# Kernel tuning notes

Hardware: AMD Instinct MI355X
Metric: run time of the kernel (lower is better)

## Reference

```python
import jax, jax.numpy as jnp
import numpy as np

DIM = 1024
HEADS = 16
HIDDEN = 4096
EPS = 1e-5


def layernorm(x, w, b):
    mu = jnp.mean(x, axis=-1, keepdims=True)
    var = jnp.var(x, axis=-1, keepdims=True)
    return (x - mu) * jax.lax.rsqrt(var + EPS) * w + b


def setup_inputs() -> dict:
    key = jax.random.key(0)
    ks = jax.random.split(key, 12)
    s = lambda fan_in: 1.0 / np.sqrt(fan_in)
    return {
        "x": jax.random.normal(ks[0], (8, 1024, DIM), dtype=jnp.float32),
        "norm1_w": jnp.ones((DIM,), jnp.float32),
        "norm1_b": jnp.zeros((DIM,), jnp.float32),
        "qkv_w": jax.random.uniform(ks[1], (3 * DIM, DIM), jnp.float32, -s(DIM), s(DIM)),
        "proj_w": jax.random.uniform(ks[2], (DIM, DIM), jnp.float32, -s(DIM), s(DIM)),
        "proj_b": jax.random.uniform(ks[3], (DIM,), jnp.float32, -s(DIM), s(DIM)),
        "norm2_w": jnp.ones((DIM,), jnp.float32),
        "norm2_b": jnp.zeros((DIM,), jnp.float32),
        "fc1_w": jax.random.uniform(ks[4], (HIDDEN, DIM), jnp.float32, -s(DIM), s(DIM)),
        "fc1_b": jax.random.uniform(ks[5], (HIDDEN,), jnp.float32, -s(DIM), s(DIM)),
        "fc2_w": jax.random.uniform(ks[6], (DIM, HIDDEN), jnp.float32, -s(HIDDEN), s(HIDDEN)),
        "fc2_b": jax.random.uniform(ks[7], (DIM,), jnp.float32, -s(HIDDEN), s(HIDDEN)),
    }


def reference(x, norm1_w, norm1_b, qkv_w, proj_w, proj_b,
              norm2_w, norm2_b, fc1_w, fc1_b, fc2_w, fc2_b):
    B, N, C = x.shape
    hd = C // HEADS
    scale = hd ** -0.5

    # ---- attention branch ----
    xn = layernorm(x, norm1_w, norm1_b)
    qkv_tmp = jnp.einsum('bnc,oc->bno', xn, qkv_w)          # [B,N,3C]
    qkv = qkv_tmp.reshape(B, N, 3, HEADS, hd).transpose(2, 0, 3, 1, 4)
    q, k, v = qkv[0], qkv[1], qkv[2]                         # [B,H,N,hd]
    qkv_out = qkv_tmp.reshape(B, N, 3, C).transpose(2, 0, 1, 3)
    attn = jnp.einsum('bhnd,bhmd->bhnm', q, k) * scale       # [B,H,N,N]
    attn = jax.nn.softmax(attn, axis=-1)
    ao = jnp.einsum('bhnm,bhmd->bhnd', attn, v)              # [B,H,N,hd]
    ao = ao.transpose(0, 2, 1, 3).reshape(B, N, C)
    attn_out = jnp.einsum('bnc,oc->bno', ao, proj_w) + proj_b
    x = x + attn_out

    # ---- mlp branch ----
    xn2 = layernorm(x, norm2_w, norm2_b)
    h = jnp.einsum('bnc,hc->bnh', xn2, fc1_w) + fc1_b
    h = jax.nn.gelu(h, approximate=False)
    hidden_out = jnp.einsum('bnh,ch->bnc', h, fc2_w) + fc2_b
    x = x + hidden_out
    return (x, (qkv_out[0], qkv_out[1], qkv_out[2]), hidden_out)
```

## Files before the change

### kernel.cpp

```cpp
#include <hip/hip_runtime.h>
#include <hip/hip_bf16.h>

typedef __attribute__((ext_vector_type(8))) __bf16 bf16x8;
typedef __attribute__((ext_vector_type(4))) float f32x4;
typedef unsigned short u16;
typedef unsigned int u32;

#define TOK 8192
#define C_DIM 1024
#define OUT_SEC 8388608

__device__ __forceinline__ u16 f2bf(float f) {
  return __builtin_bit_cast(u16, __float2bfloat16(f));
}

__device__ __forceinline__ void gl_lds16(const void* g, void* l) {
  __builtin_amdgcn_global_load_lds(
      (__attribute__((address_space(1))) void*)const_cast<void*>(g),
      (__attribute__((address_space(3))) void*)l, 16, 0, 0);
}

__device__ __forceinline__ float gelu_f(float x) {
  float y = 0.7978845608f * (x + 0.044715f * x * x * x);
  y = fminf(fmaxf(y, -15.f), 15.f);
  float e = __expf(2.0f * y);
  float th = (e - 1.0f) / (e + 1.0f);
  return 0.5f * x * (1.0f + th);
}

__global__ __launch_bounds__(256) void cvt_kernel(const float* __restrict__ in,
                                                  u16* __restrict__ out, int n4) {
  int i = blockIdx.x * blockDim.x + threadIdx.x;
  if (i >= n4) return;
  float4 v = reinterpret_cast<const float4*>(in)[i];
  alignas(8) u16 pk[4];
  pk[0] = f2bf(v.x); pk[1] = f2bf(v.y); pk[2] = f2bf(v.z); pk[3] = f2bf(v.w);
  reinterpret_cast<uint2*>(out)[i] = *reinterpret_cast<uint2*>(pk);
}

__global__ __launch_bounds__(256) void ln_kernel(const float* __restrict__ x,
                                                 const float* __restrict__ w,
                                                 const float* __restrict__ b,
                                                 u16* __restrict__ out) {
  const int row = blockIdx.x;
  const int t = threadIdx.x;
  const float* xr = x + (size_t)row * C_DIM;
  float4 v = reinterpret_cast<const float4*>(xr)[t];
  float s = v.x + v.y + v.z + v.w;
  float ss = v.x * v.x + v.y * v.y + v.z * v.z + v.w * v.w;
#pragma unroll
  for (int off = 1; off < 64; off <<= 1) {
    s += __shfl_xor(s, off, 64);
    ss += __shfl_xor(ss, off, 64);
  }
  __shared__ float red[8];
  const int wv = t >> 6;
  if ((t & 63) == 0) { red[wv] = s; red[4 + wv] = ss; }
  __syncthreads();
  s = red[0] + red[1] + red[2] + red[3];
  ss = red[4] + red[5] + red[6] + red[7];
  const float mu = s * (1.0f / C_DIM);
  const float var = ss * (1.0f / C_DIM) - mu * mu;
  const float rstd = rsqrtf(var + 1e-5f);
  float4 w4 = reinterpret_cast<const float4*>(w)[t];
  float4 b4 = reinterpret_cast<const float4*>(b)[t];
  alignas(8) u16 pk[4];
  pk[0] = f2bf((v.x - mu) * rstd * w4.x + b4.x);
  pk[1] = f2bf((v.y - mu) * rstd * w4.y + b4.y);
  pk[2] = f2bf((v.z - mu) * rstd * w4.z + b4.z);
  pk[3] = f2bf((v.w - mu) * rstd * w4.w + b4.w);
  reinterpret_cast<uint2*>(out + (size_t)row * C_DIM)[t] = *reinterpret_cast<uint2*>(pk);
}

__global__ __launch_bounds__(256) void vtrans_kernel(const float* __restrict__ vsrc,
                                                     u16* __restrict__ vt) {
  const int bh = blockIdx.x, nt = blockIdx.y;
  const int b = bh >> 4, h = bh & 15;
  const int t = threadIdx.x;
  __shared__ u16 T[64][65];
#pragma unroll
  for (int p = 0; p < 4; ++p) {
    const int idx = p * 256 + t;
    const int n = idx >> 4, d4 = (idx & 15) * 4;
    float4 x4 = *reinterpret_cast<const float4*>(
        vsrc + (size_t)(b * 1024 + nt * 64 + n) * 1024 + h * 64 + d4);
    T[d4 + 0][n] = f2bf(x4.x);
    T[d4 + 1][n] = f2bf(x4.y);
    T[d4 + 2][n] = f2bf(x4.z);
    T[d4 + 3][n] = f2bf(x4.w);
  }
  __syncthreads();
  const int d = t >> 2, ns = (t & 3) * 16;
  u16* dst = vt + (size_t)bh * 65536 + (size_t)d * 1024 + nt * 64 + ns;
  alignas(16) u16 tmp[16];
#pragma unroll
  for (int i = 0; i < 16; ++i) tmp[i] = T[d][ns + i];
  reinterpret_cast<uint4*>(dst)[0] = reinterpret_cast<uint4*>(tmp)[0];
  reinterpret_cast<uint4*>(dst)[1] = reinterpret_cast<uint4*>(tmp)[1];
}

enum { EPI8_QKV = 0, EPI8_FC1 = 1 };

#define MFMA_Q(BASE)                                                        \
  _Pragma("unroll") for (int nf = 0; nf < 4; ++nf) {                        \
    _Pragma("unroll") for (int mf = 0; mf < 4; ++mf)                        \
        acc[(BASE) + mf][nf] = __builtin_amdgcn_mfma_f32_16x16x32_bf16(     \
            af[mf], bfr[nf], acc[(BASE) + mf][nf], 0, 0, 0);                \
  }

template <int EPI>
__global__ __launch_bounds__(512, 2) void gemm8(
    const u16* __restrict__ A, const u16* __restrict__ Bw,
    const float* __restrict__ bias,
    float* __restrict__ out, u16* __restrict__ h1, u16* __restrict__ h2,
    int K) {
  extern __shared__ char smem[];
  const int t = threadIdx.x, lane = t & 63, wid = t >> 6;
  const int wm = wid >> 2, wn = wid & 3;

  const int nwg = gridDim.x;
  int lin = blockIdx.x;
  lin = (lin & 7) * (nwg >> 3) + (lin >> 3);
  const int brow0 = (lin & 31) * 256;
  const int bcol0 = (lin >> 5) * 256;

  const int NT = K >> 6;

  f32x4 zero = {0.f, 0.f, 0.f, 0.f};
  f32x4 acc[8][4];
#pragma unroll
  for (int m = 0; m < 8; ++m)
#pragma unroll
    for (int n = 0; n < 4; ++n) acc[m][n] = zero;

  const int src_slot = ((t & 3) ^ ((t >> 3) & 3)) * 8;
  const int srow = t >> 2;
  auto stage = [&](int buf, int mat, int ks, int ktile) {
    const u16* G = mat ? Bw : A;
    const int gr0 = mat ? bcol0 : brow0;
    const int k0 = ktile * 64 + ks * 32 + src_slot;
    char* dst = smem + ((buf << 16) | (mat << 15) | (ks << 14));
#pragma unroll
    for (int i = 0; i < 2; ++i)
      gl_lds16(G + (size_t)(gr0 + i * 128 + srow) * K + k0, dst + i * 8192 + t * 16);
  };

  const int swz16 = (((lane >> 4) ^ ((lane >> 1) & 3)) << 4);
  const int l15 = lane & 15;

  stage(0, 0, 0, 0);
  stage(0, 1, 0, 0);
  stage(0, 0, 1, 0);
  stage(0, 1, 1, 0);
  asm volatile("s_waitcnt vmcnt(4)" ::: "memory");
  __builtin_amdgcn_s_barrier();

  for (int tt = 0; tt < NT; ++tt) {
    char* As_ = smem + ((tt & 1) << 16);
    char* Bs_ = As_ + 32768;
    const int nbuf = (tt & 1) ^ 1;
    const bool pf = (tt + 1 < NT);
    bf16x8 af[4], bfr[4];

    auto LDA = [&](int MH, int KK) {
#pragma unroll
      for (int mf = 0; mf < 4; ++mf)
        af[mf] = *reinterpret_cast<const bf16x8*>(
            As_ + KK * 16384 + (wm * 128 + MH * 64 + mf * 16 + l15) * 64 + swz16);
    };
    auto LDB = [&](int KK) {
#pragma unroll
      for (int nf = 0; nf < 4; ++nf)
        bfr[nf] = *reinterpret_cast<const bf16x8*>(
            Bs_ + KK * 16384 + (wn * 64 + nf * 16 + l15) * 64 + swz16);
    };

    LDB(0);
    LDA(0, 0);
    if (pf) stage(nbuf, 0, 0, tt + 1);
    __builtin_amdgcn_s_barrier();
    asm volatile("s_waitcnt lgkmcnt(0)" ::: "memory");
    __builtin_amdgcn_sched_barrier(0);
    __builtin_amdgcn_s_setprio(1);
    MFMA_Q(0)
    __builtin_amdgcn_s_setprio(0);
    __builtin_amdgcn_s_barrier();

    LDA(1, 0);
    if (pf) {
      stage(nbuf, 1, 0, tt + 1);
      asm volatile("s_waitcnt vmcnt(4)" ::: "memory");
    } else {
      asm volatile("s_waitcnt vmcnt(0)" ::: "memory");
    }
    __builtin_amdgcn_s_barrier();
    asm volatile("s_waitcnt lgkmcnt(0)" ::: "memory");
    __builtin_amdgcn_sched_barrier(0);
    __builtin_amdgcn_s_setprio(1);
    MFMA_Q(4)
    __builtin_amdgcn_s_setprio(0);
    __builtin_amdgcn_s_barrier();

    LDB(1);
    LDA(1, 1);
    if (pf) stage(nbuf, 0, 1, tt + 1);
    __builtin_amdgcn_s_barrier();
    asm volatile("s_waitcnt lgkmcnt(0)" ::: "memory");
    __builtin_amdgcn_sched_barrier(0);
    __builtin_amdgcn_s_setprio(1);
    MFMA_Q(4)
    __builtin_amdgcn_s_setprio(0);
    __builtin_amdgcn_s_barrier();

    LDA(0, 1);
    if (pf) {
      stage(nbuf, 1, 1, tt + 1);
      asm volatile("s_waitcnt vmcnt(4)" ::: "memory");
    }
    __builtin_amdgcn_s_barrier();
    asm volatile("s_waitcnt lgkmcnt(0)" ::: "memory");
    __builtin_amdgcn_sched_barrier(0);
    __builtin_amdgcn_s_setprio(1);
    MFMA_Q(0)
    __builtin_amdgcn_s_setprio(0);
    __builtin_amdgcn_s_barrier();
  }

  const int rb = brow0 + wm * 128;
  const int cb = bcol0 + wn * 64;
#pragma unroll
  for (int m = 0; m < 8; ++m) {
#pragma unroll
    for (int n = 0; n < 4; ++n) {
      const int c = cb + n * 16 + l15;
#pragma unroll
      for (int j = 0; j < 4; ++j) {
        const int r = rb + m * 16 + (lane >> 4) * 4 + j;
        float v = acc[m][n][j];
        if constexpr (EPI == EPI8_QKV) {
          const int sec = c >> 10, cc = c & 1023;
          out[(size_t)sec * OUT_SEC + (size_t)r * 1024 + cc] = v;
          const size_t boff =
              (((size_t)(r >> 10) * 16 + (cc >> 6)) * 1024 + (r & 1023)) * 64 + (cc & 63);
          if (sec == 0) h1[boff] = f2bf(v * 0.18033688f);
          else if (sec == 1) h2[boff] = f2bf(v);
        } else {
          v += bias[c];
          h1[(size_t)r * 4096 + c] = f2bf(gelu_f(v));
        }
      }
    }
  }
}

enum { EPIN_PROJ = 0, EPIN_FC2 = 1 };

template <int EPI>
__global__ __launch_bounds__(512, 2) void gemm8n(
    const u16* __restrict__ A, const u16* __restrict__ Bw,
    const float* __restrict__ bias, const float* resid,
    float* out, float* out2_f, int K) {
  extern __shared__ char smem[];
  const int t = threadIdx.x, lane = t & 63, wid = t >> 6;
  const int wm = wid >> 2, wn = wid & 3;

  const int nwg = gridDim.x;
  int lin = blockIdx.x;
  lin = (lin & 7) * (nwg >> 3) + (lin >> 3);
  const int brow0 = (lin & 63) * 128;
  const int bcol0 = (lin >> 6) * 256;

  const int NT = K >> 6;

  f32x4 zero = {0.f, 0.f, 0.f, 0.f};
  f32x4 acc[4][4];
#pragma unroll
  for (int m = 0; m < 4; ++m)
#pragma unroll
    for (int n = 0; n < 4; ++n) acc[m][n] = zero;

  const int src_slot = ((t & 3) ^ ((t >> 3) & 3)) * 8;
  const int srow = t >> 2;
  auto stageA = [&](int buf, int ks, int ktile) {
    const int k0 = ktile * 64 + ks * 32 + src_slot;
    char* dst = smem + buf * 49152 + ks * 8192;
    gl_lds16(A + (size_t)(brow0 + srow) * K + k0, dst + t * 16);
  };
  auto stageB = [&](int buf, int ks, int ktile) {
    const int k0 = ktile * 64 + ks * 32 + src_slot;
    char* dst = smem + buf * 49152 + 16384 + ks * 16384;
#pragma unroll
    for (int i = 0; i < 2; ++i)
      gl_lds16(Bw + (size_t)(bcol0 + i * 128 + srow) * K + k0, dst + i * 8192 + t * 16);
  };

  const int swz16 = (((lane >> 4) ^ ((lane >> 1) & 3)) << 4);
  const int l15 = lane & 15;

  stageA(0, 0, 0);
  stageA(0, 1, 0);
  stageB(0, 0, 0);
  stageB(0, 1, 0);
  asm volatile("s_waitcnt vmcnt(2)" ::: "memory");
  __builtin_amdgcn_s_barrier();

  for (int tt = 0; tt < NT; ++tt) {
    char* As_ = smem + (tt & 1) * 49152;
    char* Bs_ = As_ + 16384;
    const int nbuf = (tt & 1) ^ 1;
    const bool pf = (tt + 1 < NT);
    bf16x8 af[4], bfr[4];

    auto LDA = [&](int KK) {
#pragma unroll
      for (int mf = 0; mf < 4; ++mf)
        af[mf] = *reinterpret_cast<const bf16x8*>(
            As_ + KK * 8192 + (wm * 64 + mf * 16 + l15) * 64 + swz16);
    };
    auto LDB = [&](int KK) {
#pragma unroll
      for (int nf = 0; nf < 4; ++nf)
        bfr[nf] = *reinterpret_cast<const bf16x8*>(
            Bs_ + KK * 16384 + (wn * 64 + nf * 16 + l15) * 64 + swz16);
    };

    LDA(0);
    LDB(0);
    if (pf) {
      stageA(nbuf, 0, tt + 1);
      stageA(nbuf, 1, tt + 1);
      stageB(nbuf, 0, tt + 1);
      asm volatile("s_waitcnt vmcnt(4)" ::: "memory");
    } else {
      asm volatile("s_waitcnt vmcnt(0)" ::: "memory");
    }
    __builtin_amdgcn_s_barrier();
    asm volatile("s_waitcnt lgkmcnt(0)" ::: "memory");
    __builtin_amdgcn_sched_barrier(0);
    __builtin_amdgcn_s_setprio(1);
    MFMA_Q(0)
    __builtin_amdgcn_s_setprio(0);
    __builtin_amdgcn_s_barrier();

    LDA(1);
    LDB(1);
    if (pf) {
      stageB(nbuf, 1, tt + 1);
      asm volatile("s_waitcnt vmcnt(2)" ::: "memory");
    }
    __builtin_amdgcn_s_barrier();
    asm volatile("s_waitcnt lgkmcnt(0)" ::: "memory");
    __builtin_amdgcn_sched_barrier(0);
    __builtin_amdgcn_s_setprio(1);
    MFMA_Q(0)
    __builtin_amdgcn_s_setprio(0);
    __builtin_amdgcn_s_barrier();
  }

  const int rb = brow0 + wm * 64;
  const int cb = bcol0 + wn * 64;
#pragma unroll
  for (int m = 0; m < 4; ++m) {
#pragma unroll
    for (int n = 0; n < 4; ++n) {
      const int c = cb + n * 16 + l15;
#pragma unroll
      for (int j = 0; j < 4; ++j) {
        const int r = rb + m * 16 + (lane >> 4) * 4 + j;
        float v = acc[m][n][j];
        if constexpr (EPI == EPIN_PROJ) {
          v += bias[c] + resid[(size_t)r * 1024 + c];
          out[(size_t)r * 1024 + c] = v;
        } else {
          v += bias[c];
          out[(size_t)r * 1024 + c] = v;
          out2_f[(size_t)r * 1024 + c] = resid[(size_t)r * 1024 + c] + v;
        }
      }
    }
  }
}

__global__ __launch_bounds__(256) void attn_kernel(const u16* __restrict__ Qb,
                                                   const u16* __restrict__ Kb,
                                                   const u16* __restrict__ Vtb,
                                                   u16* __restrict__ ao) {
  const int orig = blockIdx.y * gridDim.x + blockIdx.x;
  const int wid = (orig & 7) * 256 + (orig >> 3);
  const int bh = wid >> 4;
  const int qt = wid & 15;
  const int b = bh >> 4, h = bh & 15;
  const int t = threadIdx.x, lane = t & 63, wv = t >> 6;
  const int l15 = lane & 15, g = lane >> 4;

  __shared__ u16 Ks[2][4096];
  __shared__ u16 Vs[2][4096];

  const int q0 = qt * 64 + wv * 16;
  bf16x8 qf[2];
#pragma unroll
  for (int c = 0; c < 2; ++c)
    qf[c] = *reinterpret_cast<const bf16x8*>(
        Qb + (size_t)bh * 65536 + (size_t)(q0 + l15) * 64 + c * 32 + g * 8);

  f32x4 zero = {0.f, 0.f, 0.f, 0.f};
  f32x4 accO[4];
#pragma unroll
  for (int nb = 0; nb < 4; ++nb) accO[nb] = zero;
  float m = -1e30f, lrun = 0.f;

  const char* ktile0 = (const char*)(Kb + (size_t)bh * 65536);
  const char* vbase = (const char*)(Vtb + (size_t)bh * 65536);

  auto stage = [&](int buf, int kv0) {
#pragma unroll
    for (int i = 0; i < 2; ++i) {
      const int o = i * 4096 + t * 16;
      const int row = o >> 7, colb = o & 127;
      const int swz = colb ^ ((row & 7) << 4);
      gl_lds16(ktile0 + (size_t)kv0 * 128 + (size_t)row * 128 + swz, (char*)Ks[buf] + o);
      gl_lds16(vbase + (size_t)row * 2048 + (size_t)kv0 * 2 + swz, (char*)Vs[buf] + o);
    }
  };

  stage(0, 0);
  __syncthreads();
  int cur = 0;

  const int a0 = (l15 + ((g & 1) << 5)) << 2;
  const int a1 = a0 + 64;
  const bool up = (lane & 32) != 0;

  for (int tile = 0; tile < 16; ++tile) {
    if (tile < 15) stage(cur ^ 1, (tile + 1) * 64);

    f32x4 sacc[4];
#pragma unroll
    for (int jb = 0; jb < 4; ++jb) sacc[jb] = zero;
#pragma unroll
    for (int jb = 0; jb < 4; ++jb)
#pragma unroll
      for (int c = 0; c < 2; ++c) {
        const int row = jb * 16 + l15;
        const int colb = c * 64 + g * 16;
        bf16x8 kf = *reinterpret_cast<const bf16x8*>(
            (const char*)Ks[cur] + row * 128 + (colb ^ ((row & 7) << 4)));
        sacc[jb] = __builtin_amdgcn_mfma_f32_16x16x32_bf16(kf, qf[c], sacc[jb], 0, 0, 0);
      }

    float mt = sacc[0][0];
#pragma unroll
    for (int jb = 0; jb < 4; ++jb)
#pragma unroll
      for (int r = 0; r < 4; ++r) mt = fmaxf(mt, sacc[jb][r]);
    mt = fmaxf(mt, __shfl_xor(mt, 16, 64));
    mt = fmaxf(mt, __shfl_xor(mt, 32, 64));

    if (!__all(mt <= m + 8.0f)) {
      const float mn = fmaxf(m, mt);
      const float sc = exp2f(m - mn);
      lrun *= sc;
#pragma unroll
      for (int nb = 0; nb < 4; ++nb) accO[nb] *= sc;
      m = mn;
    }

    float rs = 0.f;
#pragma unroll
    for (int jb = 0; jb < 4; ++jb)
#pragma unroll
      for (int r = 0; r < 4; ++r) {
        const float p = exp2f(sacc[jb][r] - m);
        sacc[jb][r] = p;
        rs += p;
      }
    rs += __shfl_xor(rs, 16, 64);
    rs += __shfl_xor(rs, 32, 64);
    lrun += rs;

    int w[4][2];
#pragma unroll
    for (int jb = 0; jb < 4; ++jb) {
      w[jb][0] = (int)((u32)f2bf(sacc[jb][0]) | ((u32)f2bf(sacc[jb][1]) << 16));
      w[jb][1] = (int)((u32)f2bf(sacc[jb][2]) | ((u32)f2bf(sacc[jb][3]) << 16));
    }

#pragma unroll
    for (int c = 0; c < 2; ++c) {
      int lo0 = __builtin_amdgcn_ds_bpermute(a0, w[2 * c][0]);
      int hi0 = __builtin_amdgcn_ds_bpermute(a0, w[2 * c + 1][0]);
      int lo1 = __builtin_amdgcn_ds_bpermute(a0, w[2 * c][1]);
      int hi1 = __builtin_amdgcn_ds_bpermute(a0, w[2 * c + 1][1]);
      int lo2 = __builtin_amdgcn_ds_bpermute(a1, w[2 * c][0]);
      int hi2 = __builtin_amdgcn_ds_bpermute(a1, w[2 * c + 1][0]);
      int lo3 = __builtin_amdgcn_ds_bpermute(a1, w[2 * c][1]);
      int hi3 = __builtin_amdgcn_ds_bpermute(a1, w[2 * c + 1][1]);
      alignas(16) int word[4] = {up ? hi0 : lo0, up ? hi1 : lo1,
                                 up ? hi2 : lo2, up ? hi3 : lo3};
      bf16x8 pfB = *reinterpret_cast<bf16x8*>(word);
#pragma unroll
      for (int nb = 0; nb < 4; ++nb) {
        const int row = nb * 16 + l15;
        const int colb = c * 64 + g * 16;
        bf16x8 vf = *reinterpret_cast<const bf16x8*>(
            (const char*)Vs[cur] + row * 128 + (colb ^ ((row & 7) << 4)));
        accO[nb] = __builtin_amdgcn_mfma_f32_16x16x32_bf16(vf, pfB, accO[nb], 0, 0, 0);
      }
    }

    __syncthreads();
    cur ^= 1;
  }

  const float rl = __builtin_amdgcn_rcpf(lrun);
  u16* dst = ao + (size_t)(b * 1024 + q0 + l15) * 1024 + h * 64 + g * 4;
#pragma unroll
  for (int nb = 0; nb < 4; ++nb) {
    alignas(8) u16 pk[4];
#pragma unroll
    for (int j = 0; j < 4; ++j) pk[j] = f2bf(accO[nb][j] * rl);
    *reinterpret_cast<uint2*>(dst + nb * 16) = *reinterpret_cast<uint2*>(pk);
  }
}

extern "C" void kernel_launch(void* const* d_in, const int* in_sizes, int n_in,
                              void* d_out, int out_size, void* d_ws, size_t ws_size,
                              hipStream_t stream) {
  const float* x      = (const float*)d_in[0];
  const float* n1w    = (const float*)d_in[1];
  const float* n1b    = (const float*)d_in[2];
  const float* qkv_w  = (const float*)d_in[3];
  const float* proj_w = (const float*)d_in[4];
  const float* proj_b = (const float*)d_in[5];
  const float* n2w    = (const float*)d_in[6];
  const float* n2b    = (const float*)d_in[7];
  const float* fc1_w  = (const float*)d_in[8];
  const float* fc1_b  = (const float*)d_in[9];
  const float* fc2_w  = (const float*)d_in[10];
  const float* fc2_b  = (const float*)d_in[11];
  float* out = (float*)d_out;

  u16* wsb    = (u16*)d_ws;
  u16* w_qkv  = wsb;
  u16* w_proj = wsb + 3145728;
  u16* w_fc1  = wsb + 4194304;
  u16* w_fc2  = wsb + 8388608;
  u16* xn     = wsb + 12582912;
  u16* Qb     = wsb + 20971520;
  u16* Kb     = wsb + 29360128;
  u16* Vtw    = wsb + 37748736;
  u16* ao     = wsb + 46137344;
  u16* hbuf   = wsb + 20971520;

  (void)hipFuncSetAttribute((const void*)gemm8<EPI8_QKV>,
                            hipFuncAttributeMaxDynamicSharedMemorySize, 131072);
  (void)hipFuncSetAttribute((const void*)gemm8<EPI8_FC1>,
                            hipFuncAttributeMaxDynamicSharedMemorySize, 131072);
  (void)hipFuncSetAttribute((const void*)gemm8n<EPIN_PROJ>,
                            hipFuncAttributeMaxDynamicSharedMemorySize, 98304);
  (void)hipFuncSetAttribute((const void*)gemm8n<EPIN_FC2>,
                            hipFuncAttributeMaxDynamicSharedMemorySize, 98304);

  cvt_kernel<<<3072, 256, 0, stream>>>(qkv_w, w_qkv, 786432);
  cvt_kernel<<<1024, 256, 0, stream>>>(proj_w, w_proj, 262144);
  cvt_kernel<<<4096, 256, 0, stream>>>(fc1_w, w_fc1, 1048576);
  cvt_kernel<<<4096, 256, 0, stream>>>(fc2_w, w_fc2, 1048576);

  ln_kernel<<<TOK, 256, 0, stream>>>(x, n1w, n1b, xn);
  gemm8<EPI8_QKV><<<384, 512, 131072, stream>>>(
      xn, w_qkv, nullptr, out + OUT_SEC, Qb, Kb, 1024);
  vtrans_kernel<<<dim3(128, 16), 256, 0, stream>>>(out + 3 * (size_t)OUT_SEC, Vtw);
  attn_kernel<<<dim3(128, 16), 256, 0, stream>>>(Qb, Kb, Vtw, ao);
  gemm8n<EPIN_PROJ><<<256, 512, 98304, stream>>>(
      ao, w_proj, proj_b, x, out, nullptr, 1024);
  ln_kernel<<<TOK, 256, 0, stream>>>(out, n2w, n2b, xn);
  gemm8<EPI8_FC1><<<512, 512, 131072, stream>>>(
      xn, w_fc1, fc1_b, nullptr, hbuf, nullptr, 1024);
  gemm8n<EPIN_FC2><<<256, 512, 98304, stream>>>(
      hbuf, w_fc2, fc2_b, out, out + 4 * (size_t)OUT_SEC, out, 4096);
}
```

Baseline: 470.4 us.

## Triple-buffer LDS staging in gemm8n to prefetch two k-tiles ahead

The proj and fc2 GEMMs move from double to triple-buffered LDS, issuing the global-to-LDS loads for tile tt+2 while computing tile tt. This gives memory latency more time to hide and replaces the split prefetch with rotating buffer pointers. LDS per block grows to 144KB and launch bounds drop to one block per CU, so occupancy is lower in exchange for deeper prefetch.

```diff
diff --git a/kernel.cpp b/kernel.cpp
--- a/kernel.cpp
+++ b/kernel.cpp
@@ -256,7 +256,7 @@
 enum { EPIN_PROJ = 0, EPIN_FC2 = 1 };
 
 template <int EPI>
-__global__ __launch_bounds__(512, 2) void gemm8n(
+__global__ __launch_bounds__(512, 1) void gemm8n(
     const u16* __restrict__ A, const u16* __restrict__ Bw,
     const float* __restrict__ bias, const float* resid,
     float* out, float* out2_f, int K) {
@@ -281,59 +281,54 @@
 
   const int src_slot = ((t & 3) ^ ((t >> 3) & 3)) * 8;
   const int srow = t >> 2;
-  auto stageA = [&](int buf, int ks, int ktile) {
-    const int k0 = ktile * 64 + ks * 32 + src_slot;
-    char* dst = smem + buf * 49152 + ks * 8192;
-    gl_lds16(A + (size_t)(brow0 + srow) * K + k0, dst + t * 16);
-  };
-  auto stageB = [&](int buf, int ks, int ktile) {
-    const int k0 = ktile * 64 + ks * 32 + src_slot;
-    char* dst = smem + buf * 49152 + 16384 + ks * 16384;
-#pragma unroll
-    for (int i = 0; i < 2; ++i)
-      gl_lds16(Bw + (size_t)(bcol0 + i * 128 + srow) * K + k0, dst + i * 8192 + t * 16);
+  auto stage_all = [&](char* dst, int ktile) {
+#pragma unroll
+    for (int ks = 0; ks < 2; ++ks) {
+      const int k0 = ktile * 64 + ks * 32 + src_slot;
+      gl_lds16(A + (size_t)(brow0 + srow) * K + k0, dst + ks * 8192 + t * 16);
+    }
+#pragma unroll
+    for (int ks = 0; ks < 2; ++ks) {
+      const int k0 = ktile * 64 + ks * 32 + src_slot;
+      char* db = dst + 16384 + ks * 16384;
+#pragma unroll
+      for (int i = 0; i < 2; ++i)
+        gl_lds16(Bw + (size_t)(bcol0 + i * 128 + srow) * K + k0, db + i * 8192 + t * 16);
+    }
   };
 
   const int swz16 = (((lane >> 4) ^ ((lane >> 1) & 3)) << 4);
   const int l15 = lane & 15;
 
-  stageA(0, 0, 0);
-  stageA(0, 1, 0);
-  stageB(0, 0, 0);
-  stageB(0, 1, 0);
-  asm volatile("s_waitcnt vmcnt(2)" ::: "memory");
+  char* bcur = smem;
+  char* bnxt = smem + 49152;
+  char* bspr = smem + 98304;
+
+  stage_all(bcur, 0);
+  stage_all(bnxt, 1);
+  asm volatile("s_waitcnt vmcnt(6)" ::: "memory");
   __builtin_amdgcn_s_barrier();
 
   for (int tt = 0; tt < NT; ++tt) {
-    char* As_ = smem + (tt & 1) * 49152;
-    char* Bs_ = As_ + 16384;
-    const int nbuf = (tt & 1) ^ 1;
-    const bool pf = (tt + 1 < NT);
+    const bool pf2 = (tt + 2 < NT);
     bf16x8 af[4], bfr[4];
 
     auto LDA = [&](int KK) {
 #pragma unroll
       for (int mf = 0; mf < 4; ++mf)
         af[mf] = *reinterpret_cast<const bf16x8*>(
-            As_ + KK * 8192 + (wm * 64 + mf * 16 + l15) * 64 + swz16);
+            bcur + KK * 8192 + (wm * 64 + mf * 16 + l15) * 64 + swz16);
     };
     auto LDB = [&](int KK) {
 #pragma unroll
       for (int nf = 0; nf < 4; ++nf)
         bfr[nf] = *reinterpret_cast<const bf16x8*>(
-            Bs_ + KK * 16384 + (wn * 64 + nf * 16 + l15) * 64 + swz16);
+            bcur + 16384 + KK * 16384 + (wn * 64 + nf * 16 + l15) * 64 + swz16);
     };
 
     LDA(0);
     LDB(0);
-    if (pf) {
-      stageA(nbuf, 0, tt + 1);
-      stageA(nbuf, 1, tt + 1);
-      stageB(nbuf, 0, tt + 1);
-      asm volatile("s_waitcnt vmcnt(4)" ::: "memory");
-    } else {
-      asm volatile("s_waitcnt vmcnt(0)" ::: "memory");
-    }
+    if (pf2) stage_all(bspr, tt + 2);
     __builtin_amdgcn_s_barrier();
     asm volatile("s_waitcnt lgkmcnt(0)" ::: "memory");
     __builtin_amdgcn_sched_barrier(0);
@@ -344,9 +339,10 @@
 
     LDA(1);
     LDB(1);
-    if (pf) {
-      stageB(nbuf, 1, tt + 1);
-      asm volatile("s_waitcnt vmcnt(2)" ::: "memory");
+    if (pf2) {
+      asm volatile("s_waitcnt vmcnt(6)" ::: "memory");
+    } else {
+      asm volatile("s_waitcnt vmcnt(0)" ::: "memory");
     }
     __builtin_amdgcn_s_barrier();
     asm volatile("s_waitcnt lgkmcnt(0)" ::: "memory");
@@ -355,6 +351,11 @@
     MFMA_Q(0)
     __builtin_amdgcn_s_setprio(0);
     __builtin_amdgcn_s_barrier();
+
+    char* tmp = bcur;
+    bcur = bnxt;
+    bnxt = bspr;
+    bspr = tmp;
   }
 
   const int rb = brow0 + wm * 64;
@@ -557,9 +558,9 @@
   (void)hipFuncSetAttribute((const void*)gemm8<EPI8_FC1>,
                             hipFuncAttributeMaxDynamicSharedMemorySize, 131072);
   (void)hipFuncSetAttribute((const void*)gemm8n<EPIN_PROJ>,
-                            hipFuncAttributeMaxDynamicSharedMemorySize, 98304);
+                            hipFuncAttributeMaxDynamicSharedMemorySize, 147456);
   (void)hipFuncSetAttribute((const void*)gemm8n<EPIN_FC2>,
-                            hipFuncAttributeMaxDynamicSharedMemorySize, 98304);
+                            hipFuncAttributeMaxDynamicSharedMemorySize, 147456);
 
   cvt_kernel<<<3072, 256, 0, stream>>>(qkv_w, w_qkv, 786432);
   cvt_kernel<<<1024, 256, 0, stream>>>(proj_w, w_proj, 262144);
@@ -571,11 +572,11 @@
       xn, w_qkv, nullptr, out + OUT_SEC, Qb, Kb, 1024);
   vtrans_kernel<<<dim3(128, 16), 256, 0, stream>>>(out + 3 * (size_t)OUT_SEC, Vtw);
   attn_kernel<<<dim3(128, 16), 256, 0, stream>>>(Qb, Kb, Vtw, ao);
-  gemm8n<EPIN_PROJ><<<256, 512, 98304, stream>>>(
+  gemm8n<EPIN_PROJ><<<256, 512, 147456, stream>>>(
       ao, w_proj, proj_b, x, out, nullptr, 1024);
   ln_kernel<<<TOK, 256, 0, stream>>>(out, n2w, n2b, xn);
   gemm8<EPI8_FC1><<<512, 512, 131072, stream>>>(
       xn, w_fc1, fc1_b, nullptr, hbuf, nullptr, 1024);
-  gemm8n<EPIN_FC2><<<256, 512, 98304, stream>>>(
+  gemm8n<EPIN_FC2><<<256, 512, 147456, stream>>>(
       hbuf, w_fc2, fc2_b, out, out + 4 * (size_t)OUT_SEC, out, 4096);
 }
```

Result: no change. 473.0 us (+0.5%).
